# Kernel tuning notes

Hardware: AMD Instinct MI355X
Metric: run time of the kernel (lower is better)

Reference implementation:

```python
import jax, jax.numpy as jnp
import numpy as np

B, CIN, H, W = 1024, 1, 200, 32   # batch, in_channels, feat_nums, embed_dim
COUT = 16                          # out_channels
K = 3                              # con_kernel (height)
TOPK = 50                          # min(feat_nums, topk)
# ZeroPad2d padding for kernel (K,1): width (0,0), height (K//2 + K - 2*(K//2) - 1, K//2)
PAD_TOP = K // 2 + K - 2 * (K // 2) - 1
PAD_BOT = K // 2


def setup_inputs() -> dict:
    key = jax.random.key(0)
    k1, k2, k3 = jax.random.split(key, 3)
    x = jax.random.normal(k1, (B, CIN, H, W), dtype=jnp.float32)
    conv_w = jax.random.normal(k2, (COUT, CIN, K, 1), dtype=jnp.float32) * 0.1
    conv_b = jax.random.normal(k3, (COUT,), dtype=jnp.float32) * 0.1
    return {"x": x, "conv_w": conv_w, "conv_b": conv_b}


def reference(x, conv_w, conv_b):
    # 'same' conv along H only (kernel width is 1), stride 1
    y = jax.lax.conv_general_dilated(
        x, conv_w,
        window_strides=(1, 1),
        padding=((PAD_TOP, PAD_BOT), (0, 0)),
        dimension_numbers=("NCHW", "OIHW", "NCHW"),
    )
    y = jnp.tanh(y + conv_b[None, :, None, None])  # [B, COUT, H, W]
    # top-k along H (dim 2), values sorted descending (matches torch.topk)
    yt = jnp.swapaxes(y, 2, 3)                      # [B, COUT, W, H]
    vals, _ = jax.lax.top_k(yt, TOPK)               # [B, COUT, W, TOPK]
    return jnp.swapaxes(vals, 2, 3)                 # [B, COUT, TOPK, W]
```

## Files before the change

kernel.cpp:

```cpp
#include <hip/hip_runtime.h>
#include <math.h>

#define B_     1024
#define H_     200
#define W_     32
#define COUT_  16
#define TOPK_  50

#define XST 17
#define OST 17

typedef _Float16 h2 __attribute__((ext_vector_type(2)));
union HU { h2 h; int i; };


constexpr unsigned long long lmask(int d, int Kb) {
    unsigned long long m = 0;
    for (int l = 0; l < 64; ++l) {
        int ln = l & 15;
        bool a = (ln & d) != 0;
        bool b = Kb && ((ln & Kb) != 0);
        if (a != b) m |= (1ull << l);
    }
    return m;
}

#define XOP_1(o,v) "v_mov_b32_dpp " o ", " v " quad_perm:[1,0,3,2] row_mask:0xf bank_mask:0xf\n\t"
#define XOP_2(o,v) "v_mov_b32_dpp " o ", " v " quad_perm:[2,3,0,1] row_mask:0xf bank_mask:0xf\n\t"
#define XOP_8(o,v) "v_mov_b32_dpp " o ", " v " row_ror:8 row_mask:0xf bank_mask:0xf\n\t"
#define XOP_4(o,v) "ds_swizzle_b32 " o ", " v " offset:0x101F\n\t"
#define PRE_1 "s_nop 4\n\t"
#define PRE_2 "s_nop 4\n\t"
#define PRE_8 "s_nop 4\n\t"
#define PRE_4 ""
#define WAIT_1 ""
#define WAIT_2 ""
#define WAIT_8 ""
#define WAIT_4 "s_waitcnt lgkmcnt(0)\n\t"

#define P1_MX "v_pk_max_f16 "
#define P1_MN "v_pk_min_f16 "
#define P2_MX "v_pk_min_f16 "
#define P2_MN "v_pk_max_f16 "
#define OP_(ph,t,x,o) ph##_##t x ", " x ", " o "\n\t"

#define SRT12(d, Kb, t0,t1,t2,t3,t4,t5,t6,t7,t8,t9,tA,tB) { \
  constexpr unsigned long long M_ = lmask(d, Kb); \
  int o0,o1,o2,o3,o4,o5,o6,o7,o8,o9,oA,oB; \
  asm volatile( PRE_##d \
    XOP_##d("%[o0]","%[x0]") XOP_##d("%[o1]","%[x1]") \
    XOP_##d("%[o2]","%[x2]") XOP_##d("%[o3]","%[x3]") \
    XOP_##d("%[o4]","%[x4]") XOP_##d("%[o5]","%[x5]") \
    XOP_##d("%[o6]","%[x6]") XOP_##d("%[o7]","%[x7]") \
    XOP_##d("%[o8]","%[x8]") XOP_##d("%[o9]","%[x9]") \
    XOP_##d("%[oA]","%[xA]") XOP_##d("%[oB]","%[xB]") \
    WAIT_##d \
    "s_mov_b64 exec, %[m]\n\t" \
    OP_(P1,t0,"%[x0]","%[o0]") OP_(P1,t1,"%[x1]","%[o1]") \
    OP_(P1,t2,"%[x2]","%[o2]") OP_(P1,t3,"%[x3]","%[o3]") \
    OP_(P1,t4,"%[x4]","%[o4]") OP_(P1,t5,"%[x5]","%[o5]") \
    OP_(P1,t6,"%[x6]","%[o6]") OP_(P1,t7,"%[x7]","%[o7]") \
    OP_(P1,t8,"%[x8]","%[o8]") OP_(P1,t9,"%[x9]","%[o9]") \
    OP_(P1,tA,"%[xA]","%[oA]") OP_(P1,tB,"%[xB]","%[oB]") \
    "s_not_b64 exec, exec\n\t" \
    OP_(P2,t0,"%[x0]","%[o0]") OP_(P2,t1,"%[x1]","%[o1]") \
    OP_(P2,t2,"%[x2]","%[o2]") OP_(P2,t3,"%[x3]","%[o3]") \
    OP_(P2,t4,"%[x4]","%[o4]") OP_(P2,t5,"%[x5]","%[o5]") \
    OP_(P2,t6,"%[x6]","%[o6]") OP_(P2,t7,"%[x7]","%[o7]") \
    OP_(P2,t8,"%[x8]","%[o8]") OP_(P2,t9,"%[x9]","%[o9]") \
    OP_(P2,tA,"%[xA]","%[oA]") OP_(P2,tB,"%[xB]","%[oB]") \
    "s_mov_b64 exec, -1\n\t" \
    : [x0]"+v"(a0),[x1]"+v"(a1),[x2]"+v"(a2),[x3]"+v"(a3), \
      [x4]"+v"(b0),[x5]"+v"(b1),[x6]"+v"(b2),[x7]"+v"(b3), \
      [x8]"+v"(e0),[x9]"+v"(e1),[xA]"+v"(e2),[xB]"+v"(e3), \
      [o0]"=&v"(o0),[o1]"=&v"(o1),[o2]"=&v"(o2),[o3]"=&v"(o3), \
      [o4]"=&v"(o4),[o5]"=&v"(o5),[o6]"=&v"(o6),[o7]"=&v"(o7), \
      [o8]"=&v"(o8),[o9]"=&v"(o9),[oA]"=&v"(oA),[oB]"=&v"(oB) \
    : [m]"s"(M_)); }

#define SRT_A(d,Kb) SRT12(d,Kb, MX,MX,MX,MX, MN,MN,MN,MN, MX,MX,MX,MX)
#define SRT_B(d)    SRT12(d,0,  MX,MN,MX,MN, MN,MX,MN,MX, MX,MN,MX,MN)
#define SRT_C(d)    SRT12(d,0,  MX,MX,MN,MN, MN,MN,MX,MX, MX,MX,MN,MN)

#define C3(d, Kb) { constexpr unsigned long long M_ = lmask(d, Kb); int oF; \
  asm volatile( PRE_##d XOP_##d("%[oF]","%[xF]") WAIT_##d \
    "s_mov_b64 exec, %[m]\n\t" \
    "v_pk_min_f16 %[xF], %[xF], %[oF]\n\t" \
    "s_not_b64 exec, exec\n\t" \
    "v_pk_max_f16 %[xF], %[xF], %[oF]\n\t" \
    "s_mov_b64 exec, -1\n\t" \
    : [xF]"+v"(f0), [oF]"=&v"(oF) : [m]"s"(M_)); }

#define MRG8(d) { constexpr unsigned long long M_ = lmask(d, 0); \
  int o0,o1,o2,o3,o4,o5,o6,o7; \
  asm volatile( PRE_##d \
    XOP_##d("%[o0]","%[x0]") XOP_##d("%[o1]","%[x1]") \
    XOP_##d("%[o2]","%[x2]") XOP_##d("%[o3]","%[x3]") \
    XOP_##d("%[o4]","%[x4]") XOP_##d("%[o5]","%[x5]") \
    XOP_##d("%[o6]","%[x6]") XOP_##d("%[o7]","%[x7]") \
    WAIT_##d \
    "s_mov_b64 exec, %[m]\n\t" \
    "v_pk_max_f16 %[x0], %[x0], %[o0]\n\t" \
    "v_pk_max_f16 %[x1], %[x1], %[o1]\n\t" \
    "v_pk_max_f16 %[x2], %[x2], %[o2]\n\t" \
    "v_pk_max_f16 %[x3], %[x3], %[o3]\n\t" \
    "v_pk_min_f16 %[x4], %[x4], %[o4]\n\t" \
    "v_pk_min_f16 %[x5], %[x5], %[o5]\n\t" \
    "v_pk_min_f16 %[x6], %[x6], %[o6]\n\t" \
    "v_pk_min_f16 %[x7], %[x7], %[o7]\n\t" \
    "s_not_b64 exec, exec\n\t" \
    "v_pk_min_f16 %[x0], %[x0], %[o0]\n\t" \
    "v_pk_min_f16 %[x1], %[x1], %[o1]\n\t" \
    "v_pk_min_f16 %[x2], %[x2], %[o2]\n\t" \
    "v_pk_min_f16 %[x3], %[x3], %[o3]\n\t" \
    "v_pk_max_f16 %[x4], %[x4], %[o4]\n\t" \
    "v_pk_max_f16 %[x5], %[x5], %[o5]\n\t" \
    "v_pk_max_f16 %[x6], %[x6], %[o6]\n\t" \
    "v_pk_max_f16 %[x7], %[x7], %[o7]\n\t" \
    "s_mov_b64 exec, -1\n\t" \
    : [x0]"+v"(g0),[x1]"+v"(g1),[x2]"+v"(g2),[x3]"+v"(g3), \
      [x4]"+v"(e0),[x5]"+v"(e1),[x6]"+v"(e2),[x7]"+v"(e3), \
      [o0]"=&v"(o0),[o1]"=&v"(o1),[o2]"=&v"(o2),[o3]"=&v"(o3), \
      [o4]"=&v"(o4),[o5]"=&v"(o5),[o6]"=&v"(o6),[o7]"=&v"(o7) \
    : [m]"s"(M_)); }

#define FIN4(d) { constexpr unsigned long long M_ = lmask(d, 0); \
  int o0,o1,o2,o3; \
  asm volatile( PRE_##d \
    XOP_##d("%[o0]","%[x0]") XOP_##d("%[o1]","%[x1]") \
    XOP_##d("%[o2]","%[x2]") XOP_##d("%[o3]","%[x3]") \
    WAIT_##d \
    "s_mov_b64 exec, %[m]\n\t" \
    "v_pk_min_f16 %[x0], %[x0], %[o0]\n\t" \
    "v_pk_min_f16 %[x1], %[x1], %[o1]\n\t" \
    "v_pk_min_f16 %[x2], %[x2], %[o2]\n\t" \
    "v_pk_min_f16 %[x3], %[x3], %[o3]\n\t" \
    "s_not_b64 exec, exec\n\t" \
    "v_pk_max_f16 %[x0], %[x0], %[o0]\n\t" \
    "v_pk_max_f16 %[x1], %[x1], %[o1]\n\t" \
    "v_pk_max_f16 %[x2], %[x2], %[o2]\n\t" \
    "v_pk_max_f16 %[x3], %[x3], %[o3]\n\t" \
    "s_mov_b64 exec, -1\n\t" \
    : [x0]"+v"(g0),[x1]"+v"(g1),[x2]"+v"(g2),[x3]"+v"(g3), \
      [o0]"=&v"(o0),[o1]"=&v"(o1),[o2]"=&v"(o2),[o3]"=&v"(o3) \
    : [m]"s"(M_)); }

__device__ __forceinline__ int pkmx(int a, int b) {
    int r; asm("v_pk_max_f16 %0, %1, %2" : "=v"(r) : "v"(a), "v"(b)); return r;
}
__device__ __forceinline__ int pkmn(int a, int b) {
    int r; asm("v_pk_min_f16 %0, %1, %2" : "=v"(r) : "v"(a), "v"(b)); return r;
}
#define RCE(A,B,FLIP) { int mn_ = pkmn(A,B), mx_ = pkmx(A,B); \
  if (FLIP) { A = mx_; B = mn_; } else { A = mn_; B = mx_; } }

__device__ __forceinline__ float fast_tanh(float s) {
    float e = __expf(2.0f * s);
    return fmaf(-2.0f, __builtin_amdgcn_rcpf(e + 1.0f), 1.0f);
}

__global__ __launch_bounds__(256, 8) void cnn_topk_kernel(
    const float* __restrict__ x,
    const float* __restrict__ cw,
    const float* __restrict__ cb,
    float* __restrict__ out)
{
    __shared__ float xs[(H_ + 2) * XST];
    __shared__ int   obuf[TOPK_ * OST];

    const int b   = blockIdx.x >> 1;
    const int wh  = blockIdx.x & 1;
    const int tid = threadIdx.x;
    const float* xb = x + (size_t)b * (H_ * W_) + wh * 16;

    for (int i = tid; i < H_ * 4; i += 256) {
        int h = i >> 2, q = (i & 3) * 4;
        float4 v = *reinterpret_cast<const float4*>(xb + h * W_ + q);
        float* d = &xs[(h + 1) * XST + q];
        d[0] = v.x; d[1] = v.y; d[2] = v.z; d[3] = v.w;
    }
    if (tid < 16) {
        xs[tid] = 0.0f;
        xs[(H_ + 1) * XST + tid] = 0.0f;
    }
    __syncthreads();

    const int wave = tid >> 6;
    const int lane = tid & 63;
    const int ln   = lane & 15;
    const int col  = wave * 4 + (lane >> 4);

    const int SENT = (int)0xFC00FC00;
    const bool tail_ok = (ln < 8);
    const int h3t = (192 + ln < H_) ? (192 + ln) : (H_ - 1);
    const float* xsf = &xs[ln * XST + col];
    const float* xst = &xs[h3t * XST + col];
    int* obase = &obuf[ln * OST + col];

#pragma unroll 1
    for (int cp = 0; cp < 8; ++cp) {
        const int coA = 2 * cp, coB = 2 * cp + 1;
        const float w0A = cw[coA * 3], w1A = cw[coA * 3 + 1], w2A = cw[coA * 3 + 2], bA = cb[coA];
        const float w0B = cw[coB * 3], w1B = cw[coB * 3 + 1], w2B = cw[coB * 3 + 2], bB = cb[coB];

        int a0,a1,a2,a3,b0,b1,b2,b3,e0,e1,e2,e3,f0;
#define CONV1(VR, CO) { \
        float xm = xsf[(CO)*XST], xc = xsf[((CO)+1)*XST], xp = xsf[((CO)+2)*XST]; \
        float sA = fmaf(w2A, xp, fmaf(w1A, xc, fmaf(w0A, xm, bA))); \
        float sB = fmaf(w2B, xp, fmaf(w1B, xc, fmaf(w0B, xm, bB))); \
        VR = __builtin_bit_cast(int, __builtin_amdgcn_cvt_pkrtz(sA, sB)); }
        CONV1(a0, 0)   CONV1(a1, 16)  CONV1(a2, 32)  CONV1(a3, 48)
        CONV1(b0, 64)  CONV1(b1, 80)  CONV1(b2, 96)  CONV1(b3, 112)
        CONV1(e0, 128) CONV1(e1, 144) CONV1(e2, 160) CONV1(e3, 176)
        { float xm = xst[0], xc = xst[XST], xp = xst[2*XST];
          float sA = fmaf(w2A, xp, fmaf(w1A, xc, fmaf(w0A, xm, bA)));
          float sB = fmaf(w2B, xp, fmaf(w1B, xc, fmaf(w0B, xm, bB)));
          int vt = __builtin_bit_cast(int, __builtin_amdgcn_cvt_pkrtz(sA, sB));
          f0 = tail_ok ? vt : SENT; }
#undef CONV1

        SRT_A(1, 2)
        SRT_A(2, 4) SRT_A(1, 4)
        SRT_A(4, 8) SRT_A(2, 8) SRT_A(1, 8)
        SRT_B(8) SRT_B(4) SRT_B(2) SRT_B(1)
        RCE(a0,a1,0) RCE(a2,a3,1) RCE(b0,b1,1) RCE(b2,b3,0) RCE(e0,e1,0) RCE(e2,e3,1)
        SRT_C(8) SRT_C(4) SRT_C(2) SRT_C(1)
        RCE(a0,a2,0) RCE(a1,a3,0) RCE(b0,b2,1) RCE(b1,b3,1) RCE(e0,e2,0) RCE(e1,e3,0)
        RCE(a0,a1,0) RCE(a2,a3,0) RCE(b0,b1,1) RCE(b2,b3,1) RCE(e0,e1,0) RCE(e2,e3,0)
        SRT_A(8, 0) SRT_A(4, 0) SRT_A(2, 0) SRT_A(1, 0)

        C3(1, 2) C3(2, 4) C3(1, 4) C3(4, 0) C3(2, 0) C3(1, 0)

        int g0 = pkmx(a0, b0), g1 = pkmx(a1, b1), g2 = pkmx(a2, b2), g3 = pkmx(a3, b3);
        e0 = pkmx(e0, f0);
        RCE(g0,g2,0) RCE(g1,g3,0) RCE(e0,e2,1) RCE(e1,e3,1)
        RCE(g0,g1,0) RCE(g2,g3,0) RCE(e0,e1,1) RCE(e2,e3,1)
        MRG8(8) MRG8(4) MRG8(2) MRG8(1)
        g0 = pkmx(g0, e0); g1 = pkmx(g1, e1); g2 = pkmx(g2, e2); g3 = pkmx(g3, e3);
        RCE(g0,g2,1) RCE(g1,g3,1)
        RCE(g0,g1,1) RCE(g2,g3,1)
        FIN4(8) FIN4(4) FIN4(2) FIN4(1)

        obase[0]            = g0;
        obase[16 * OST]     = g1;
        obase[32 * OST]     = g2;
        if (ln < 2) obase[48 * OST] = g3;
        __syncthreads();

#pragma unroll
        for (int j = 0; j < 4; ++j) {
            int idx = tid + j * 256;
            if (idx < 800) {
                int k = idx >> 4, w2 = idx & 15;
                HU u; u.i = obuf[k * OST + w2];
                size_t o0 = (((size_t)b * COUT_ + coA) * TOPK_ + k) * W_ + wh * 16 + w2;
                out[o0]                        = fast_tanh((float)u.h.x);
                out[o0 + (size_t)TOPK_ * W_]   = fast_tanh((float)u.h.y);
            }
        }
        __syncthreads();
    }
}

extern "C" void kernel_launch(void* const* d_in, const int* in_sizes, int n_in,
                              void* d_out, int out_size, void* d_ws, size_t ws_size,
                              hipStream_t stream) {
    const float* x  = (const float*)d_in[0];
    const float* cw = (const float*)d_in[1];
    const float* cb = (const float*)d_in[2];
    float* out = (float*)d_out;

    cnn_topk_kernel<<<dim3(B_ * 2), dim3(256), 0, stream>>>(x, cw, cb, out);
}
```

Before: 230.0 us.

## Transpose shared input tile to column-major and use ds_swizzle for lane exchanges

Stores the input tile in shared memory as [column][height] with a 208-element stride, so each lane's three conv taps are consecutive addresses. The xor-2 and xor-8 lane exchanges in the sorting network switch from DPP moves to ds_swizzle, replacing s_nop hazards with lgkmcnt waits. The intent is to change the LDS access pattern and instruction scheduling. In exchange, the fill loop now does scattered scalar stores, and swizzle goes through the LDS path with higher latency.

```diff
diff --git a/kernel.cpp b/kernel.cpp
--- a/kernel.cpp
+++ b/kernel.cpp
@@ -7,7 +7,7 @@
 #define COUT_  16
 #define TOPK_  50
 
-#define XST 17
+#define CST 208
 #define OST 17
 
 typedef _Float16 h2 __attribute__((ext_vector_type(2)));
@@ -26,17 +26,17 @@
 }
 
 #define XOP_1(o,v) "v_mov_b32_dpp " o ", " v " quad_perm:[1,0,3,2] row_mask:0xf bank_mask:0xf\n\t"
-#define XOP_2(o,v) "v_mov_b32_dpp " o ", " v " quad_perm:[2,3,0,1] row_mask:0xf bank_mask:0xf\n\t"
-#define XOP_8(o,v) "v_mov_b32_dpp " o ", " v " row_ror:8 row_mask:0xf bank_mask:0xf\n\t"
+#define XOP_2(o,v) "ds_swizzle_b32 " o ", " v " offset:0x081F\n\t"
 #define XOP_4(o,v) "ds_swizzle_b32 " o ", " v " offset:0x101F\n\t"
+#define XOP_8(o,v) "ds_swizzle_b32 " o ", " v " offset:0x201F\n\t"
 #define PRE_1 "s_nop 4\n\t"
-#define PRE_2 "s_nop 4\n\t"
-#define PRE_8 "s_nop 4\n\t"
+#define PRE_2 ""
 #define PRE_4 ""
+#define PRE_8 ""
 #define WAIT_1 ""
-#define WAIT_2 ""
-#define WAIT_8 ""
+#define WAIT_2 "s_waitcnt lgkmcnt(0)\n\t"
 #define WAIT_4 "s_waitcnt lgkmcnt(0)\n\t"
+#define WAIT_8 "s_waitcnt lgkmcnt(0)\n\t"
 
 #define P1_MX "v_pk_max_f16 "
 #define P1_MN "v_pk_min_f16 "
@@ -165,7 +165,7 @@
     const float* __restrict__ cb,
     float* __restrict__ out)
 {
-    __shared__ float xs[(H_ + 2) * XST];
+    __shared__ float xs[16 * CST];
     __shared__ int   obuf[TOPK_ * OST];
 
     const int b   = blockIdx.x >> 1;
@@ -174,14 +174,16 @@
     const float* xb = x + (size_t)b * (H_ * W_) + wh * 16;
 
     for (int i = tid; i < H_ * 4; i += 256) {
-        int h = i >> 2, q = (i & 3) * 4;
-        float4 v = *reinterpret_cast<const float4*>(xb + h * W_ + q);
-        float* d = &xs[(h + 1) * XST + q];
-        d[0] = v.x; d[1] = v.y; d[2] = v.z; d[3] = v.w;
+        int h = i >> 2, qg = (i & 3) * 4;
+        float4 v = *reinterpret_cast<const float4*>(xb + h * W_ + qg);
+        xs[(qg + 0) * CST + h + 1] = v.x;
+        xs[(qg + 1) * CST + h + 1] = v.y;
+        xs[(qg + 2) * CST + h + 1] = v.z;
+        xs[(qg + 3) * CST + h + 1] = v.w;
     }
     if (tid < 16) {
-        xs[tid] = 0.0f;
-        xs[(H_ + 1) * XST + tid] = 0.0f;
+        xs[tid * CST] = 0.0f;
+        xs[tid * CST + H_ + 1] = 0.0f;
     }
     __syncthreads();
 
@@ -193,8 +195,8 @@
     const int SENT = (int)0xFC00FC00;
     const bool tail_ok = (ln < 8);
     const int h3t = (192 + ln < H_) ? (192 + ln) : (H_ - 1);
-    const float* xsf = &xs[ln * XST + col];
-    const float* xst = &xs[h3t * XST + col];
+    const float* xsf = &xs[col * CST + ln];
+    const float* xst = &xs[col * CST + h3t];
     int* obase = &obuf[ln * OST + col];
 
 #pragma unroll 1
@@ -205,14 +207,14 @@
 
         int a0,a1,a2,a3,b0,b1,b2,b3,e0,e1,e2,e3,f0;
 #define CONV1(VR, CO) { \
-        float xm = xsf[(CO)*XST], xc = xsf[((CO)+1)*XST], xp = xsf[((CO)+2)*XST]; \
+        float xm = xsf[(CO)], xc = xsf[(CO)+1], xp = xsf[(CO)+2]; \
         float sA = fmaf(w2A, xp, fmaf(w1A, xc, fmaf(w0A, xm, bA))); \
         float sB = fmaf(w2B, xp, fmaf(w1B, xc, fmaf(w0B, xm, bB))); \
         VR = __builtin_bit_cast(int, __builtin_amdgcn_cvt_pkrtz(sA, sB)); }
         CONV1(a0, 0)   CONV1(a1, 16)  CONV1(a2, 32)  CONV1(a3, 48)
         CONV1(b0, 64)  CONV1(b1, 80)  CONV1(b2, 96)  CONV1(b3, 112)
         CONV1(e0, 128) CONV1(e1, 144) CONV1(e2, 160) CONV1(e3, 176)
-        { float xm = xst[0], xc = xst[XST], xp = xst[2*XST];
+        { float xm = xst[0], xc = xst[1], xp = xst[2];
           float sA = fmaf(w2A, xp, fmaf(w1A, xc, fmaf(w0A, xm, bA)));
           float sB = fmaf(w2B, xp, fmaf(w1B, xc, fmaf(w0B, xm, bB)));
           int vt = __builtin_bit_cast(int, __builtin_amdgcn_cvt_pkrtz(sA, sB));
```

Result: faster. 218.5 us (-5.0%).
